# Performance work log

Measured on AMD Instinct MI355X. Metric: run time of the kernel, lower is better.

The kernel has to match this reference:

```python
import jax, jax.numpy as jnp
import numpy as np

B, S, D, H, T, R = 2, 2048, 768, 12, 64, 50
DH = D // H
EPS = 1e-12


def setup_inputs() -> dict:
    key = jax.random.key(0)
    ks = jax.random.split(key, 12)
    w = lambda k, shape: jax.random.normal(k, shape, jnp.float32) * 0.02
    inp = {
        "hidden_states": jax.random.normal(ks[0], (B, S, D), jnp.float32),
        "tag_emb": w(ks[1], (T, D)),
        "sa_wq": w(ks[2], (D, D)), "sa_bq": jnp.zeros((D,), jnp.float32),
        "sa_wk": w(ks[3], (D, D)), "sa_bk": jnp.zeros((D,), jnp.float32),
        "sa_wv": w(ks[4], (D, D)), "sa_bv": jnp.zeros((D,), jnp.float32),
        "sa_wo": w(ks[5], (D, D)), "sa_bo": jnp.zeros((D,), jnp.float32),
        "sa_ln_g": jnp.ones((D,), jnp.float32), "sa_ln_b": jnp.zeros((D,), jnp.float32),
        "ca_wq": w(ks[6], (D, D)), "ca_bq": jnp.zeros((D,), jnp.float32),
        "ca_wk": w(ks[7], (D, D)), "ca_bk": jnp.zeros((D,), jnp.float32),
        "ca_wv": w(ks[8], (D, D)), "ca_bv": jnp.zeros((D,), jnp.float32),
        "ca_wo": w(ks[9], (D, D)), "ca_bo": jnp.zeros((D,), jnp.float32),
        "ca_ln_g": jnp.ones((D,), jnp.float32), "ca_ln_b": jnp.zeros((D,), jnp.float32),
        "ff_w1": w(ks[10], (D, 3072)), "ff_b1": jnp.zeros((3072,), jnp.float32),
        "ff_w2": w(ks[11], (3072, D)), "ff_b2": jnp.zeros((D,), jnp.float32),
        "ff_ln_g": jnp.ones((D,), jnp.float32), "ff_ln_b": jnp.zeros((D,), jnp.float32),
    }
    return inp


def _layernorm(x, g, b):
    m = jnp.mean(x, axis=-1, keepdims=True)
    v = jnp.mean(jnp.square(x - m), axis=-1, keepdims=True)
    return (x - m) * jax.lax.rsqrt(v + EPS) * g + b


def _bert_attention(x, kv, mask, wq, bq, wk, bk, wv, bv, wo, bo, ln_g, ln_b):
    # BertSelfAttention: multi-head attn; mask (if any) is ADDED to scores (HF semantics).
    Bq, Sq = x.shape[0], x.shape[1]
    Sk = kv.shape[1]
    q = (x @ wq + bq).reshape(Bq, Sq, H, DH)
    k = (kv @ wk + bk).reshape(Bq, Sk, H, DH)
    v = (kv @ wv + bv).reshape(Bq, Sk, H, DH)
    scores = jnp.einsum("bqhd,bkhd->bhqk", q, k) / jnp.sqrt(jnp.float32(DH))
    if mask is not None:
        scores = scores + mask  # additive 0/1 band mask, as in the source
    probs = jax.nn.softmax(scores, axis=-1)
    ctx = jnp.einsum("bhqk,bkhd->bqhd", probs, v).reshape(Bq, Sq, D)
    # BertSelfOutput: dense + residual + LayerNorm
    return _layernorm(ctx @ wo + bo + x, ln_g, ln_b)


def reference(hidden_states, tag_emb,
              sa_wq, sa_bq, sa_wk, sa_bk, sa_wv, sa_bv, sa_wo, sa_bo, sa_ln_g, sa_ln_b,
              ca_wq, ca_bq, ca_wk, ca_bk, ca_wv, ca_bv, ca_wo, ca_bo, ca_ln_g, ca_ln_b,
              ff_w1, ff_b1, ff_w2, ff_b2, ff_ln_g, ff_ln_b):
    Sd = hidden_states.shape[1]
    # banded mask: tril(+R) * triu(-R) -> 1 inside window, 0 outside (added to scores)
    i = jnp.arange(Sd)
    band = (jnp.abs(i[:, None] - i[None, :]) <= R).astype(hidden_states.dtype)  # [S,S]
    attn_out = _bert_attention(hidden_states, hidden_states, band,
                               sa_wq, sa_bq, sa_wk, sa_bk, sa_wv, sa_bv,
                               sa_wo, sa_bo, sa_ln_g, sa_ln_b)
    tags = jnp.broadcast_to(tag_emb[None], (hidden_states.shape[0], T, D))
    attn_out = _bert_attention(attn_out, tags, None,
                               ca_wq, ca_bq, ca_wk, ca_bk, ca_wv, ca_bv,
                               ca_wo, ca_bo, ca_ln_g, ca_ln_b)
    # BertIntermediate + BertOutput (exact erf gelu as in HF)
    inter = jax.nn.gelu(attn_out @ ff_w1 + ff_b1, approximate=False)
    return _layernorm(inter @ ff_w2 + ff_b2 + attn_out, ff_ln_g, ff_ln_b)
```

## Files before the change

### kernel.cpp

```cpp
#include <hip/hip_runtime.h>
#include <cstdint>
#include <cstddef>


typedef __bf16 bf16;
typedef __bf16 bf16x8 __attribute__((ext_vector_type(8)));
typedef __bf16 bf16x4 __attribute__((ext_vector_type(4)));
typedef __bf16 bf16x2 __attribute__((ext_vector_type(2)));
typedef float  floatx4 __attribute__((ext_vector_type(4)));

__device__ __forceinline__ void glds16(const bf16* g, bf16* l) {
  __builtin_amdgcn_global_load_lds((const __attribute__((address_space(1))) void*)g,
                                   (__attribute__((address_space(3))) void*)l, 16, 0, 0);
}

__device__ __forceinline__ float fexp2(float x) {
  float r;
  asm("v_exp_f32 %0, %1" : "=v"(r) : "v"(x));
  return r;
}

__global__ __launch_bounds__(256) void k_concat3(const float* __restrict__ a,
                                                 const float* __restrict__ b,
                                                 const float* __restrict__ c,
                                                 float* __restrict__ o, int seg) {
  int i = blockIdx.x * 256 + threadIdx.x;
  int s = i / seg, j = i - s * seg;
  const float* p = s == 0 ? a : (s == 1 ? b : c);
  o[i] = p[j];
}

__global__ void k_pad_tags(const float* __restrict__ tag, bf16* __restrict__ out) {
  int i = blockIdx.x * 256 + threadIdx.x;
  if (i < 64 * 768) out[i] = (bf16)tag[i];
  else if (i < 128 * 768) out[i] = (bf16)0.f;
}

__global__ __launch_bounds__(256) void k_transpose(const float* __restrict__ W,
                                                   bf16* __restrict__ Wt,
                                                   int K, int N) {
  __shared__ bf16 tile[64][72];
  int n0 = blockIdx.x * 64, k0 = blockIdx.y * 64;
  int t = threadIdx.x;
  int r = t >> 2, cg = (t & 3) * 16;
  const float* src = W + (size_t)(k0 + r) * N + n0 + cg;
  float tmp[16];
  *(float4*)&tmp[0]  = *(const float4*)(src);
  *(float4*)&tmp[4]  = *(const float4*)(src + 4);
  *(float4*)&tmp[8]  = *(const float4*)(src + 8);
  *(float4*)&tmp[12] = *(const float4*)(src + 12);
#pragma unroll
  for (int i = 0; i < 16; ++i) tile[r][cg + i] = (bf16)tmp[i];
  __syncthreads();
  bf16* dst = Wt + (size_t)(n0 + r) * K + k0 + cg;
#pragma unroll
  for (int g = 0; g < 2; ++g) {
    bf16x8 pack;
#pragma unroll
    for (int i = 0; i < 8; ++i) pack[i] = tile[cg + g * 8 + i][r];
    *(bf16x8*)(dst + g * 8) = pack;
  }
}

__global__ __launch_bounds__(256) void k_transpose4(const float* __restrict__ W0,
                                                    const float* __restrict__ W1,
                                                    const float* __restrict__ W2w,
                                                    const float* __restrict__ W3,
                                                    bf16* __restrict__ Wt) {
  __shared__ bf16 tile[64][72];
  int z = blockIdx.z;
  const float* W = z == 0 ? W0 : (z == 1 ? W1 : (z == 2 ? W2w : W3));
  bf16* dstb = Wt + (size_t)z * 768 * 768;
  int n0 = blockIdx.x * 64, k0 = blockIdx.y * 64;
  int t = threadIdx.x;
  int r = t >> 2, cg = (t & 3) * 16;
  const float* src = W + (size_t)(k0 + r) * 768 + n0 + cg;
  float tmp[16];
  *(float4*)&tmp[0]  = *(const float4*)(src);
  *(float4*)&tmp[4]  = *(const float4*)(src + 4);
  *(float4*)&tmp[8]  = *(const float4*)(src + 8);
  *(float4*)&tmp[12] = *(const float4*)(src + 12);
#pragma unroll
  for (int i = 0; i < 16; ++i) tile[r][cg + i] = (bf16)tmp[i];
  __syncthreads();
  bf16* dst = dstb + (size_t)(n0 + r) * 768 + k0 + cg;
#pragma unroll
  for (int g = 0; g < 2; ++g) {
    bf16x8 pack;
#pragma unroll
    for (int i = 0; i < 8; ++i) pack[i] = tile[cg + g * 8 + i][r];
    *(bf16x8*)(dst + g * 8) = pack;
  }
}

template <int BM, int BN, int KS, bool AF32, bool CF32>
__global__ __launch_bounds__(256) void k_gemm(const void* __restrict__ Av,
                                              const bf16* __restrict__ Bt,
                                              const float* __restrict__ bias,
                                              void* __restrict__ Cv,
                                              void* __restrict__ Cv2,
                                              int M, int N, int K, int ld, int act) {
  constexpr int MT = BM / 32;
  constexpr int NT = BN / 32;
  __shared__ bf16 As[KS][BM * 32];
  __shared__ bf16 Bs[KS][BN * 32];
  int tid = threadIdx.x;
  int lane = tid & 63, wave = tid >> 6;
  int l16 = lane & 15, quad = lane >> 4;
  int wm = wave & 1, wn = wave >> 1;
  int m0 = blockIdx.x * BM, n0 = blockIdx.y * BN;
  int z = blockIdx.z;
  int arow = tid >> 2, acol = (tid & 3) * 8;
  int ldst = arow * 32 + acol;

  const bf16* Ab = (const bf16*)Av;
  const float* Af = (const float*)Av;
  const bf16* Ap = Ab + (size_t)(m0 + arow) * ld + z * K + acol;
  const float* Apf = Af + (size_t)(m0 + arow) * ld + acol;
  const bf16* Bp = Bt + (size_t)(n0 + arow) * ld + z * K + acol;

  floatx4 acc[MT][NT];
#pragma unroll
  for (int i = 0; i < MT; ++i)
#pragma unroll
    for (int j = 0; j < NT; ++j) acc[i][j] = floatx4{0.f, 0.f, 0.f, 0.f};

  float4 p0a, p0b, p1a, p1b;
  if constexpr (AF32) {
    p0a = *(const float4*)(Apf);
    p0b = *(const float4*)(Apf + 4);
    if constexpr (BM == 128) {
      p1a = *(const float4*)(Apf + (size_t)64 * ld);
      p1b = *(const float4*)(Apf + (size_t)64 * ld + 4);
    }
  }

  for (int k = 0; k < K; k += 32 * KS) {
    __syncthreads();
#pragma unroll
    for (int ks = 0; ks < KS; ++ks) {
      glds16(Bp + k + ks * 32, &Bs[ks][ldst]);
      if constexpr (BN == 128) glds16(Bp + (size_t)64 * ld + k + ks * 32, &Bs[ks][ldst + 2048]);
    }
    if constexpr (AF32) {
      bf16x8 c0;
      c0[0] = (bf16)p0a.x; c0[1] = (bf16)p0a.y; c0[2] = (bf16)p0a.z; c0[3] = (bf16)p0a.w;
      c0[4] = (bf16)p0b.x; c0[5] = (bf16)p0b.y; c0[6] = (bf16)p0b.z; c0[7] = (bf16)p0b.w;
      *(bf16x8*)&As[0][ldst] = c0;
      if constexpr (BM == 128) {
        bf16x8 c1;
        c1[0] = (bf16)p1a.x; c1[1] = (bf16)p1a.y; c1[2] = (bf16)p1a.z; c1[3] = (bf16)p1a.w;
        c1[4] = (bf16)p1b.x; c1[5] = (bf16)p1b.y; c1[6] = (bf16)p1b.z; c1[7] = (bf16)p1b.w;
        *(bf16x8*)&As[0][ldst + 2048] = c1;
      }
    } else {
#pragma unroll
      for (int ks = 0; ks < KS; ++ks) {
        glds16(Ap + k + ks * 32, &As[ks][ldst]);
        if constexpr (BM == 128) glds16(Ap + (size_t)64 * ld + k + ks * 32, &As[ks][ldst + 2048]);
      }
    }
    __syncthreads();
    if constexpr (AF32) {
      if (k + 32 < K) {
        p0a = *(const float4*)(Apf + k + 32);
        p0b = *(const float4*)(Apf + k + 36);
        if constexpr (BM == 128) {
          p1a = *(const float4*)(Apf + (size_t)64 * ld + k + 32);
          p1b = *(const float4*)(Apf + (size_t)64 * ld + k + 36);
        }
      }
    }
#pragma unroll
    for (int ks = 0; ks < KS; ++ks) {
      bf16x8 a_frag[MT], b_frag[NT];
#pragma unroll
      for (int mt = 0; mt < MT; ++mt)
        a_frag[mt] = *(const bf16x8*)&As[ks][(wm * (BM / 2) + mt * 16 + l16) * 32 + quad * 8];
#pragma unroll
      for (int nt = 0; nt < NT; ++nt)
        b_frag[nt] = *(const bf16x8*)&Bs[ks][(wn * (BN / 2) + nt * 16 + l16) * 32 + quad * 8];
#pragma unroll
      for (int mt = 0; mt < MT; ++mt)
#pragma unroll
        for (int nt = 0; nt < NT; ++nt)
          acc[mt][nt] = __builtin_amdgcn_mfma_f32_16x16x32_bf16(a_frag[mt], b_frag[nt], acc[mt][nt], 0, 0, 0);
    }
  }

  void* Co = (z == 0) ? Cv : Cv2;
#pragma unroll
  for (int nt = 0; nt < NT; ++nt) {
    int col = n0 + wn * (BN / 2) + nt * 16 + l16;
    float bv = (z == 0) ? bias[col] : 0.f;
#pragma unroll
    for (int mt = 0; mt < MT; ++mt) {
#pragma unroll
      for (int r = 0; r < 4; ++r) {
        int row = m0 + wm * (BM / 2) + mt * 16 + quad * 4 + r;
        float v = acc[mt][nt][r] + bv;
        if (act) v = 0.5f * v * (1.f + erff(v * 0.70710678118654752f));
        if constexpr (CF32) ((float*)Co)[(size_t)row * N + col] = v;
        else ((bf16*)Co)[(size_t)row * N + col] = (bf16)v;
      }
    }
  }
}

__global__ __launch_bounds__(256) void k_attn_mfma(const bf16* __restrict__ Q, int ldq,
                                                   const bf16* __restrict__ Kp,
                                                   const bf16* __restrict__ Vp, int ldkv,
                                                   bf16* __restrict__ O,
                                                   int S, int Skv,
                                                   long long kv_bstride, int bandR) {
  const int NH = 12;
  int qt = blockIdx.x, bh = blockIdx.y;
  int bb = bh / NH, h = bh % NH;
  const bf16* Qb = Q + (size_t)bb * S * ldq + h * 64;
  const bf16* Kb = Kp + (size_t)bb * kv_bstride + h * 64;
  const bf16* Vb = Vp + (size_t)bb * kv_bstride + h * 64;
  bf16* Ob = O + (size_t)bb * S * 768 + h * 64;

  __shared__ __align__(16) char smem[47104];
  float* Obuf = (float*)smem;
  float* l0_arr = (float*)(smem + 16896);

  int tid = threadIdx.x, wave = tid >> 6, lane = tid & 63;
  int quad = lane >> 4, l16 = lane & 15;
  int qh = wave & 1, kh = wave >> 1;
  bf16 (*Psw)[40] = (bf16(*)[40])(smem + 36864 + wave * 2560);

  const float C1 = 0.18033688f;
  const float C2 = 1.44269504f;

  int r = tid >> 2, cg = (tid & 3) * 16;
  int vk0 = 2 * (tid & 31);
  int vd0 = 8 * (tid >> 5);
  int vcol = (vk0 + 16 * (vd0 >> 4)) & 63;

  bf16x8 aq[2][2];
#pragma unroll
  for (int mt = 0; mt < 2; ++mt) {
    const bf16* qsrc = Qb + (size_t)(qt * 64 + qh * 32 + mt * 16 + l16) * ldq;
#pragma unroll
    for (int ks = 0; ks < 2; ++ks) {
      bf16x8 t = *(const bf16x8*)(qsrc + ks * 32 + quad * 8);
#pragma unroll
      for (int e = 0; e < 8; ++e) t[e] = (bf16)((float)t[e] * C1);
      aq[mt][ks] = t;
    }
  }

  bf16x8 kr0, kr1, vr0, vr1;
  {
    const bf16* ksrc = Kb + (size_t)r * ldkv + cg;
    kr0 = *(const bf16x8*)ksrc;
    kr1 = *(const bf16x8*)(ksrc + 8);
    const bf16* vsrc = Vb + (size_t)vk0 * ldkv + vd0;
    vr0 = *(const bf16x8*)vsrc;
    vr1 = *(const bf16x8*)(vsrc + ldkv);
  }

  float l_part[2][4];
  floatx4 acc[2][4];
#pragma unroll
  for (int mt = 0; mt < 2; ++mt)
#pragma unroll
    for (int j = 0; j < 4; ++j) {
      l_part[mt][j] = 0.f;
      acc[mt][j] = floatx4{0.f, 0.f, 0.f, 0.f};
    }

  int qi0 = qt * 64 + qh * 32 + quad * 4;

  for (int kc = 0; kc < Skv; kc += 64) {
    int cur = (kc >> 6) & 1;
    bf16 (*Ks)[72] = (bf16(*)[72])(smem + cur * 9216);
    bf16 (*Vt)[72] = (bf16(*)[72])(smem + 18432 + cur * 9216);
    *(bf16x8*)&Ks[r][cg] = kr0;
    *(bf16x8*)&Ks[r][cg + 8] = kr1;
#pragma unroll
    for (int e = 0; e < 8; ++e) {
      bf16x2 p; p[0] = vr0[e]; p[1] = vr1[e];
      *(bf16x2*)&Vt[vd0 + e][vcol] = p;
    }
    if (kc + 64 < Skv) {
      const bf16* ksrc = Kb + (size_t)(kc + 64 + r) * ldkv + cg;
      kr0 = *(const bf16x8*)ksrc;
      kr1 = *(const bf16x8*)(ksrc + 8);
      const bf16* vsrc = Vb + (size_t)(kc + 64 + vk0) * ldkv + vd0;
      vr0 = *(const bf16x8*)vsrc;
      vr1 = *(const bf16x8*)(vsrc + ldkv);
    }
    __syncthreads();

    floatx4 s[2][2];
    __builtin_amdgcn_s_setprio(1);
#pragma unroll
    for (int kt = 0; kt < 2; ++kt) {
      bf16x8 bk0 = *(const bf16x8*)&Ks[kh * 32 + kt * 16 + l16][quad * 8];
      bf16x8 bk1 = *(const bf16x8*)&Ks[kh * 32 + kt * 16 + l16][32 + quad * 8];
#pragma unroll
      for (int mt = 0; mt < 2; ++mt) {
        floatx4 c = {0.f, 0.f, 0.f, 0.f};
        c = __builtin_amdgcn_mfma_f32_16x16x32_bf16(aq[mt][0], bk0, c, 0, 0, 0);
        c = __builtin_amdgcn_mfma_f32_16x16x32_bf16(aq[mt][1], bk1, c, 0, 0, 0);
        s[mt][kt] = c;
      }
    }
    __builtin_amdgcn_s_setprio(0);

    bool masked = (bandR >= 0) && (kc <= qt * 64 + 63 + bandR) &&
                  (kc + 63 >= qt * 64 - bandR);
    if (masked) {
#pragma unroll
      for (int kt = 0; kt < 2; ++kt) {
        int kj = kc + kh * 32 + kt * 16 + l16;
        int colp = (kt * 16 + l16 + 8 * quad) & 31;
#pragma unroll
        for (int mt = 0; mt < 2; ++mt)
#pragma unroll
          for (int rr = 0; rr < 4; ++rr) {
            int d = qi0 + mt * 16 + rr - kj; if (d < 0) d = -d;
            float e = fexp2(s[mt][kt][rr] + (d <= bandR ? C2 : 0.f));
            l_part[mt][rr] += e;
            Psw[mt * 16 + quad * 4 + rr][colp] = (bf16)e;
          }
      }
    } else {
#pragma unroll
      for (int kt = 0; kt < 2; ++kt) {
        int colp = (kt * 16 + l16 + 8 * quad) & 31;
#pragma unroll
        for (int mt = 0; mt < 2; ++mt)
#pragma unroll
          for (int rr = 0; rr < 4; ++rr) {
            float e = fexp2(s[mt][kt][rr]);
            l_part[mt][rr] += e;
            Psw[mt * 16 + quad * 4 + rr][colp] = (bf16)e;
          }
      }
    }

    bf16x8 ap[2];
#pragma unroll
    for (int mt = 0; mt < 2; ++mt)
      ap[mt] = *(const bf16x8*)&Psw[mt * 16 + l16][8 * ((quad + (l16 >> 2)) & 3)];
    __builtin_amdgcn_s_setprio(1);
#pragma unroll
    for (int nt = 0; nt < 4; ++nt) {
      bf16x8 bv = *(const bf16x8*)&Vt[nt * 16 + l16][(kh * 32 + quad * 8 + 16 * nt) & 63];
#pragma unroll
      for (int mt = 0; mt < 2; ++mt)
        acc[mt][nt] = __builtin_amdgcn_mfma_f32_16x16x32_bf16(ap[mt], bv, acc[mt][nt], 0, 0, 0);
    }
    __builtin_amdgcn_s_setprio(0);
  }

  float lr[2][4];
#pragma unroll
  for (int mt = 0; mt < 2; ++mt)
#pragma unroll
    for (int rr = 0; rr < 4; ++rr) {
      float t = l_part[mt][rr];
      t += __shfl_xor(t, 1);
      t += __shfl_xor(t, 2);
      t += __shfl_xor(t, 4);
      t += __shfl_xor(t, 8);
      lr[mt][rr] = t;
    }
  __syncthreads();
  if (kh == 0) {
#pragma unroll
    for (int mt = 0; mt < 2; ++mt)
#pragma unroll
      for (int nt = 0; nt < 4; ++nt)
#pragma unroll
        for (int rr = 0; rr < 4; ++rr)
          Obuf[(qh * 32 + mt * 16 + quad * 4 + rr) * 66 + nt * 16 + l16] = acc[mt][nt][rr];
    if (l16 == 0) {
#pragma unroll
      for (int mt = 0; mt < 2; ++mt)
#pragma unroll
        for (int rr = 0; rr < 4; ++rr)
          l0_arr[qh * 32 + mt * 16 + quad * 4 + rr] = lr[mt][rr];
    }
  }
  __syncthreads();
  if (kh == 1) {
#pragma unroll
    for (int mt = 0; mt < 2; ++mt)
#pragma unroll
      for (int rr = 0; rr < 4; ++rr) {
        int ql = qh * 32 + mt * 16 + quad * 4 + rr;
        float lt = lr[mt][rr] + l0_arr[ql];
        int qrow = qt * 64 + ql;
#pragma unroll
        for (int nt = 0; nt < 4; ++nt) {
          float o = (acc[mt][nt][rr] + Obuf[ql * 66 + nt * 16 + l16]) / lt;
          Ob[(size_t)qrow * 768 + nt * 16 + l16] = (bf16)o;
        }
      }
  }
}

template <typename TY, typename TR, typename TO>
__global__ __launch_bounds__(256) void k_add_ln(const TY* __restrict__ Y,
                                                const TR* __restrict__ X,
                                                const float* __restrict__ Y2,
                                                const float* __restrict__ g,
                                                const float* __restrict__ b,
                                                TO* __restrict__ out) {
  int wave = threadIdx.x >> 6, lane = threadIdx.x & 63;
  int row = blockIdx.x * 4 + wave;
  const TY* y = Y + (size_t)row * 768;
  const TR* x = X + (size_t)row * 768;
  float v[12];
  float s = 0.f, s2 = 0.f;
#pragma unroll
  for (int c = 0; c < 3; ++c) {
    int idx = c * 256 + lane * 4;
    float yv[4], xv[4];
    if constexpr (__is_same(TY, float)) {
      float4 t = *(const float4*)(y + idx);
      yv[0] = t.x; yv[1] = t.y; yv[2] = t.z; yv[3] = t.w;
    } else {
      bf16x4 t = *(const bf16x4*)(y + idx);
#pragma unroll
      for (int i = 0; i < 4; ++i) yv[i] = (float)t[i];
    }
    if constexpr (__is_same(TR, float)) {
      float4 t = *(const float4*)(x + idx);
      xv[0] = t.x; xv[1] = t.y; xv[2] = t.z; xv[3] = t.w;
    } else {
      bf16x4 t = *(const bf16x4*)(x + idx);
#pragma unroll
      for (int i = 0; i < 4; ++i) xv[i] = (float)t[i];
    }
    if (Y2 != nullptr) {
      float4 t2 = *(const float4*)(Y2 + (size_t)row * 768 + idx);
      xv[0] += t2.x; xv[1] += t2.y; xv[2] += t2.z; xv[3] += t2.w;
    }
#pragma unroll
    for (int i = 0; i < 4; ++i) {
      float t = yv[i] + xv[i];
      v[c * 4 + i] = t; s += t; s2 += t * t;
    }
  }
#pragma unroll
  for (int off = 32; off > 0; off >>= 1) { s += __shfl_xor(s, off); s2 += __shfl_xor(s2, off); }
  float mean = s * (1.f / 768.f);
  float var = fmaxf(s2 * (1.f / 768.f) - mean * mean, 0.f);
  float inv = rsqrtf(var + 1e-12f);
  TO* o = out + (size_t)row * 768;
#pragma unroll
  for (int c = 0; c < 3; ++c) {
    int idx = c * 256 + lane * 4;
    float4 gv = *(const float4*)(g + idx);
    float4 bv = *(const float4*)(b + idx);
    float r0 = (v[c * 4 + 0] - mean) * inv * gv.x + bv.x;
    float r1 = (v[c * 4 + 1] - mean) * inv * gv.y + bv.y;
    float r2 = (v[c * 4 + 2] - mean) * inv * gv.z + bv.z;
    float r3 = (v[c * 4 + 3] - mean) * inv * gv.w + bv.w;
    if constexpr (__is_same(TO, float)) {
      float4 ov = {r0, r1, r2, r3};
      *(float4*)(o + idx) = ov;
    } else {
      bf16x4 ov;
      ov[0] = (bf16)r0; ov[1] = (bf16)r1; ov[2] = (bf16)r2; ov[3] = (bf16)r3;
      *(bf16x4*)(o + idx) = ov;
    }
  }
}

extern "C" void kernel_launch(void* const* d_in, const int* in_sizes, int n_in,
                              void* d_out, int out_size, void* d_ws, size_t ws_size,
                              hipStream_t stream) {
  (void)in_sizes; (void)n_in; (void)out_size; (void)ws_size;
  const float* X     = (const float*)d_in[0];
  const float* tag   = (const float*)d_in[1];
  const float* sa_wq = (const float*)d_in[2];
  const float* sa_bq = (const float*)d_in[3];
  const float* sa_wk = (const float*)d_in[4];
  const float* sa_bk = (const float*)d_in[5];
  const float* sa_wv = (const float*)d_in[6];
  const float* sa_bv = (const float*)d_in[7];
  const float* sa_wo = (const float*)d_in[8];
  const float* sa_bo = (const float*)d_in[9];
  const float* sa_lg = (const float*)d_in[10];
  const float* sa_lb = (const float*)d_in[11];
  const float* ca_wq = (const float*)d_in[12];
  const float* ca_bq = (const float*)d_in[13];
  const float* ca_wk = (const float*)d_in[14];
  const float* ca_bk = (const float*)d_in[15];
  const float* ca_wv = (const float*)d_in[16];
  const float* ca_bv = (const float*)d_in[17];
  const float* ca_wo = (const float*)d_in[18];
  const float* ca_bo = (const float*)d_in[19];
  const float* ca_lg = (const float*)d_in[20];
  const float* ca_lb = (const float*)d_in[21];
  const float* ff_w1 = (const float*)d_in[22];
  const float* ff_b1 = (const float*)d_in[23];
  const float* ff_w2 = (const float*)d_in[24];
  const float* ff_b2 = (const float*)d_in[25];
  const float* ff_lg = (const float*)d_in[26];
  const float* ff_lb = (const float*)d_in[27];

  float* outf = (float*)d_out;
  bf16* outb = (bf16*)d_out;
  const size_t SLOT = (size_t)4096 * 768;

  bf16* BIG   = (bf16*)d_ws;
  bf16* slotA = BIG + (size_t)4096 * 2304;
  bf16* Wall  = slotA + SLOT;
  bf16* W2    = Wall + (size_t)3072 * 768;
  bf16* tagp  = W2;
  bf16* k2v2  = W2 + (size_t)128 * 768;
  float* bQKV = (float*)(W2 + (size_t)128 * 768 + (size_t)128 * 1536);
  float* bKV2 = bQKV + 2304;
  float* P1   = (float*)(BIG + 2 * SLOT);

  dim3 blk(256);

  k_concat3<<<dim3(9), blk, 0, stream>>>(sa_bq, sa_bk, sa_bv, bQKV, 768);
  k_concat3<<<dim3(6), blk, 0, stream>>>(ca_bk, ca_bv, nullptr, bKV2, 768);
  k_pad_tags<<<dim3(384), blk, 0, stream>>>(tag, tagp);

  k_transpose4<<<dim3(12, 12, 4), blk, 0, stream>>>(sa_wq, sa_wk, sa_wv, sa_wo, Wall);
  k_gemm<64, 128, 1, true, false><<<dim3(64, 18), blk, 0, stream>>>(X, Wall, bQKV, BIG, nullptr,
                                                                    4096, 2304, 768, 768, 0);
  k_attn_mfma<<<dim3(32, 24), blk, 0, stream>>>(BIG, 2304, BIG + 768, BIG + 1536, 2304,
                                                outb, 2048, 2048, (long long)2048 * 2304, 50);
  k_gemm<64, 64, 2, false, false><<<dim3(64, 12), blk, 0, stream>>>(outb, Wall + (size_t)2304 * 768,
                                                                    sa_bo, slotA, nullptr,
                                                                    4096, 768, 768, 768, 0);
  k_add_ln<bf16, float, bf16><<<dim3(1024), blk, 0, stream>>>(slotA, X, nullptr, sa_lg, sa_lb, slotA);

  k_transpose4<<<dim3(12, 12, 4), blk, 0, stream>>>(ca_wq, ca_wk, ca_wv, ca_wo, Wall);
  k_gemm<64, 64, 2, false, false><<<dim3(64, 12), blk, 0, stream>>>(slotA, Wall, ca_bq, BIG, nullptr,
                                                                    4096, 768, 768, 768, 0);
  k_gemm<64, 64, 2, false, false><<<dim3(2, 24), blk, 0, stream>>>(tagp, Wall + (size_t)768 * 768,
                                                                   bKV2, k2v2, nullptr,
                                                                   128, 1536, 768, 768, 0);
  k_attn_mfma<<<dim3(32, 24), blk, 0, stream>>>(BIG, 768, k2v2, k2v2 + 768, 1536,
                                                outb, 2048, 64, 0, -1);
  k_gemm<64, 64, 2, false, false><<<dim3(64, 12), blk, 0, stream>>>(outb, Wall + (size_t)2304 * 768,
                                                                    ca_bo, BIG + SLOT, nullptr,
                                                                    4096, 768, 768, 768, 0);
  k_add_ln<bf16, bf16, bf16><<<dim3(1024), blk, 0, stream>>>(BIG + SLOT, slotA, nullptr,
                                                             ca_lg, ca_lb, slotA);

  k_transpose<<<dim3(48, 12), blk, 0, stream>>>(ff_w1, Wall, 768, 3072);
  k_transpose<<<dim3(12, 48), blk, 0, stream>>>(ff_w2, W2, 3072, 768);
  for (int mc = 0; mc < 2; ++mc) {
    const bf16* a2 = slotA + (size_t)mc * 2048 * 768;
    float* yo = outf + (size_t)mc * 2048 * 768;
    k_gemm<64, 128, 2, false, false><<<dim3(32, 24), blk, 0, stream>>>(a2, Wall, ff_b1, BIG, nullptr,
                                                                       2048, 3072, 768, 768, 1);
    k_gemm<64, 64, 2, false, true><<<dim3(32, 12, 2), blk, 0, stream>>>(BIG, W2, ff_b2, yo, P1,
                                                                        2048, 768, 1536, 3072, 0);
    k_add_ln<float, bf16, float><<<dim3(512), blk, 0, stream>>>(yo, a2, P1, ff_lg, ff_lb, yo);
  }
}
```

Baseline: 397.1 us.

## Precast input to bf16, merge prep kernels, deepen GEMM K-staging

Three small setup kernels are merged into one launch. A new pass converts the fp32 hidden states to bf16 up front, so the QKV GEMM can drop its register-staged fp32 A path and use direct global-to-LDS loads like the other GEMMs. All GEMMs now stage four 32-wide K slices per sync instead of one or two, and the QKV GEMM tile changes from 64x128 to 64x64. This cuts launches and barrier count per K, but adds an extra read and write of the input and uses more LDS per block, which may lower occupancy.

```diff
diff --git a/kernel.cpp b/kernel.cpp
--- a/kernel.cpp
+++ b/kernel.cpp
@@ -20,20 +20,41 @@
   return r;
 }
 
-__global__ __launch_bounds__(256) void k_concat3(const float* __restrict__ a,
-                                                 const float* __restrict__ b,
-                                                 const float* __restrict__ c,
-                                                 float* __restrict__ o, int seg) {
-  int i = blockIdx.x * 256 + threadIdx.x;
-  int s = i / seg, j = i - s * seg;
-  const float* p = s == 0 ? a : (s == 1 ? b : c);
-  o[i] = p[j];
-}
-
-__global__ void k_pad_tags(const float* __restrict__ tag, bf16* __restrict__ out) {
-  int i = blockIdx.x * 256 + threadIdx.x;
-  if (i < 64 * 768) out[i] = (bf16)tag[i];
-  else if (i < 128 * 768) out[i] = (bf16)0.f;
+__global__ __launch_bounds__(256) void k_prep(const float* __restrict__ sa_bq,
+                                              const float* __restrict__ sa_bk,
+                                              const float* __restrict__ sa_bv,
+                                              const float* __restrict__ ca_bk,
+                                              const float* __restrict__ ca_bv,
+                                              const float* __restrict__ tag,
+                                              float* __restrict__ bQKV,
+                                              float* __restrict__ bKV2,
+                                              bf16* __restrict__ tagp) {
+  int b = blockIdx.x, t = threadIdx.x;
+  if (b < 9) {
+    int i = b * 256 + t;
+    int s = i / 768, j = i - s * 768;
+    const float* p = s == 0 ? sa_bq : (s == 1 ? sa_bk : sa_bv);
+    bQKV[i] = p[j];
+  } else if (b < 15) {
+    int i = (b - 9) * 256 + t;
+    int s = i / 768, j = i - s * 768;
+    bKV2[i] = s == 0 ? ca_bk[j] : ca_bv[j];
+  } else {
+    int i = (b - 15) * 256 + t;
+    if (i < 64 * 768) tagp[i] = (bf16)tag[i];
+    else tagp[i] = (bf16)0.f;
+  }
+}
+
+__global__ __launch_bounds__(256) void k_precast(const float* __restrict__ X,
+                                                 bf16* __restrict__ Xb) {
+  int i = (blockIdx.x * 256 + threadIdx.x) * 8;
+  float4 a = *(const float4*)(X + i);
+  float4 b4 = *(const float4*)(X + i + 4);
+  bf16x8 o;
+  o[0] = (bf16)a.x; o[1] = (bf16)a.y; o[2] = (bf16)a.z; o[3] = (bf16)a.w;
+  o[4] = (bf16)b4.x; o[5] = (bf16)b4.y; o[6] = (bf16)b4.z; o[7] = (bf16)b4.w;
+  *(bf16x8*)(Xb + i) = o;
 }
 
 __global__ __launch_bounds__(256) void k_transpose(const float* __restrict__ W,
@@ -93,8 +114,8 @@
   }
 }
 
-template <int BM, int BN, int KS, bool AF32, bool CF32>
-__global__ __launch_bounds__(256) void k_gemm(const void* __restrict__ Av,
+template <int BM, int BN, int KS, bool CF32>
+__global__ __launch_bounds__(256) void k_gemm(const bf16* __restrict__ Ab,
                                               const bf16* __restrict__ Bt,
                                               const float* __restrict__ bias,
                                               void* __restrict__ Cv,
@@ -113,10 +134,7 @@
   int arow = tid >> 2, acol = (tid & 3) * 8;
   int ldst = arow * 32 + acol;
 
-  const bf16* Ab = (const bf16*)Av;
-  const float* Af = (const float*)Av;
   const bf16* Ap = Ab + (size_t)(m0 + arow) * ld + z * K + acol;
-  const float* Apf = Af + (size_t)(m0 + arow) * ld + acol;
   const bf16* Bp = Bt + (size_t)(n0 + arow) * ld + z * K + acol;
 
   floatx4 acc[MT][NT];
@@ -124,16 +142,6 @@
   for (int i = 0; i < MT; ++i)
 #pragma unroll
     for (int j = 0; j < NT; ++j) acc[i][j] = floatx4{0.f, 0.f, 0.f, 0.f};
-
-  float4 p0a, p0b, p1a, p1b;
-  if constexpr (AF32) {
-    p0a = *(const float4*)(Apf);
-    p0b = *(const float4*)(Apf + 4);
-    if constexpr (BM == 128) {
-      p1a = *(const float4*)(Apf + (size_t)64 * ld);
-      p1b = *(const float4*)(Apf + (size_t)64 * ld + 4);
-    }
-  }
 
   for (int k = 0; k < K; k += 32 * KS) {
     __syncthreads();
@@ -141,36 +149,10 @@
     for (int ks = 0; ks < KS; ++ks) {
       glds16(Bp + k + ks * 32, &Bs[ks][ldst]);
       if constexpr (BN == 128) glds16(Bp + (size_t)64 * ld + k + ks * 32, &Bs[ks][ldst + 2048]);
-    }
-    if constexpr (AF32) {
-      bf16x8 c0;
-      c0[0] = (bf16)p0a.x; c0[1] = (bf16)p0a.y; c0[2] = (bf16)p0a.z; c0[3] = (bf16)p0a.w;
-      c0[4] = (bf16)p0b.x; c0[5] = (bf16)p0b.y; c0[6] = (bf16)p0b.z; c0[7] = (bf16)p0b.w;
-      *(bf16x8*)&As[0][ldst] = c0;
-      if constexpr (BM == 128) {
-        bf16x8 c1;
-        c1[0] = (bf16)p1a.x; c1[1] = (bf16)p1a.y; c1[2] = (bf16)p1a.z; c1[3] = (bf16)p1a.w;
-        c1[4] = (bf16)p1b.x; c1[5] = (bf16)p1b.y; c1[6] = (bf16)p1b.z; c1[7] = (bf16)p1b.w;
-        *(bf16x8*)&As[0][ldst + 2048] = c1;
-      }
-    } else {
-#pragma unroll
-      for (int ks = 0; ks < KS; ++ks) {
-        glds16(Ap + k + ks * 32, &As[ks][ldst]);
-        if constexpr (BM == 128) glds16(Ap + (size_t)64 * ld + k + ks * 32, &As[ks][ldst + 2048]);
-      }
+      glds16(Ap + k + ks * 32, &As[ks][ldst]);
+      if constexpr (BM == 128) glds16(Ap + (size_t)64 * ld + k + ks * 32, &As[ks][ldst + 2048]);
     }
     __syncthreads();
-    if constexpr (AF32) {
-      if (k + 32 < K) {
-        p0a = *(const float4*)(Apf + k + 32);
-        p0b = *(const float4*)(Apf + k + 36);
-        if constexpr (BM == 128) {
-          p1a = *(const float4*)(Apf + (size_t)64 * ld + k + 32);
-          p1b = *(const float4*)(Apf + (size_t)64 * ld + k + 36);
-        }
-      }
-    }
 #pragma unroll
     for (int ks = 0; ks < KS; ++ks) {
       bf16x8 a_frag[MT], b_frag[NT];
@@ -519,34 +501,35 @@
   float* bQKV = (float*)(W2 + (size_t)128 * 768 + (size_t)128 * 1536);
   float* bKV2 = bQKV + 2304;
   float* P1   = (float*)(BIG + 2 * SLOT);
+  bf16*  Xb   = outb + SLOT;
 
   dim3 blk(256);
 
-  k_concat3<<<dim3(9), blk, 0, stream>>>(sa_bq, sa_bk, sa_bv, bQKV, 768);
-  k_concat3<<<dim3(6), blk, 0, stream>>>(ca_bk, ca_bv, nullptr, bKV2, 768);
-  k_pad_tags<<<dim3(384), blk, 0, stream>>>(tag, tagp);
+  k_prep<<<dim3(399), blk, 0, stream>>>(sa_bq, sa_bk, sa_bv, ca_bk, ca_bv, tag,
+                                        bQKV, bKV2, tagp);
+  k_precast<<<dim3(1536), blk, 0, stream>>>(X, Xb);
 
   k_transpose4<<<dim3(12, 12, 4), blk, 0, stream>>>(sa_wq, sa_wk, sa_wv, sa_wo, Wall);
-  k_gemm<64, 128, 1, true, false><<<dim3(64, 18), blk, 0, stream>>>(X, Wall, bQKV, BIG, nullptr,
-                                                                    4096, 2304, 768, 768, 0);
+  k_gemm<64, 64, 4, false><<<dim3(64, 36), blk, 0, stream>>>(Xb, Wall, bQKV, BIG, nullptr,
+                                                             4096, 2304, 768, 768, 0);
   k_attn_mfma<<<dim3(32, 24), blk, 0, stream>>>(BIG, 2304, BIG + 768, BIG + 1536, 2304,
                                                 outb, 2048, 2048, (long long)2048 * 2304, 50);
-  k_gemm<64, 64, 2, false, false><<<dim3(64, 12), blk, 0, stream>>>(outb, Wall + (size_t)2304 * 768,
-                                                                    sa_bo, slotA, nullptr,
-                                                                    4096, 768, 768, 768, 0);
+  k_gemm<64, 64, 4, false><<<dim3(64, 12), blk, 0, stream>>>(outb, Wall + (size_t)2304 * 768,
+                                                             sa_bo, slotA, nullptr,
+                                                             4096, 768, 768, 768, 0);
   k_add_ln<bf16, float, bf16><<<dim3(1024), blk, 0, stream>>>(slotA, X, nullptr, sa_lg, sa_lb, slotA);
 
   k_transpose4<<<dim3(12, 12, 4), blk, 0, stream>>>(ca_wq, ca_wk, ca_wv, ca_wo, Wall);
-  k_gemm<64, 64, 2, false, false><<<dim3(64, 12), blk, 0, stream>>>(slotA, Wall, ca_bq, BIG, nullptr,
-                                                                    4096, 768, 768, 768, 0);
-  k_gemm<64, 64, 2, false, false><<<dim3(2, 24), blk, 0, stream>>>(tagp, Wall + (size_t)768 * 768,
-                                                                   bKV2, k2v2, nullptr,
-                                                                   128, 1536, 768, 768, 0);
+  k_gemm<64, 64, 4, false><<<dim3(64, 12), blk, 0, stream>>>(slotA, Wall, ca_bq, BIG, nullptr,
+                                                             4096, 768, 768, 768, 0);
+  k_gemm<64, 64, 4, false><<<dim3(2, 24), blk, 0, stream>>>(tagp, Wall + (size_t)768 * 768,
+                                                            bKV2, k2v2, nullptr,
+                                                            128, 1536, 768, 768, 0);
   k_attn_mfma<<<dim3(32, 24), blk, 0, stream>>>(BIG, 768, k2v2, k2v2 + 768, 1536,
                                                 outb, 2048, 64, 0, -1);
-  k_gemm<64, 64, 2, false, false><<<dim3(64, 12), blk, 0, stream>>>(outb, Wall + (size_t)2304 * 768,
-                                                                    ca_bo, BIG + SLOT, nullptr,
-                                                                    4096, 768, 768, 768, 0);
+  k_gemm<64, 64, 4, false><<<dim3(64, 12), blk, 0, stream>>>(outb, Wall + (size_t)2304 * 768,
+                                                             ca_bo, BIG + SLOT, nullptr,
+                                                             4096, 768, 768, 768, 0);
   k_add_ln<bf16, bf16, bf16><<<dim3(1024), blk, 0, stream>>>(BIG + SLOT, slotA, nullptr,
                                                              ca_lg, ca_lb, slotA);
 
@@ -555,10 +538,10 @@
   for (int mc = 0; mc < 2; ++mc) {
     const bf16* a2 = slotA + (size_t)mc * 2048 * 768;
     float* yo = outf + (size_t)mc * 2048 * 768;
-    k_gemm<64, 128, 2, false, false><<<dim3(32, 24), blk, 0, stream>>>(a2, Wall, ff_b1, BIG, nullptr,
-                                                                       2048, 3072, 768, 768, 1);
-    k_gemm<64, 64, 2, false, true><<<dim3(32, 12, 2), blk, 0, stream>>>(BIG, W2, ff_b2, yo, P1,
-                                                                        2048, 768, 1536, 3072, 0);
+    k_gemm<64, 128, 4, false><<<dim3(32, 24), blk, 0, stream>>>(a2, Wall, ff_b1, BIG, nullptr,
+                                                                2048, 3072, 768, 768, 1);
+    k_gemm<64, 64, 4, true><<<dim3(32, 12, 2), blk, 0, stream>>>(BIG, W2, ff_b2, yo, P1,
+                                                                 2048, 768, 1536, 3072, 0);
     k_add_ln<float, bf16, float><<<dim3(512), blk, 0, stream>>>(yo, a2, P1, ff_lg, ff_lb, yo);
   }
 }
```

New measurement: 397.4 us. No clear change (+0.1%).
